# Kernel tuning notes

Measured on AMD Instinct MI355X. Metric: run time of the kernel, lower is better.

Reference implementation:

```python
import jax, jax.numpy as jnp
import numpy as np

Q, K, H, W, D, N, DFF = 48, 48, 24, 8, 512, 3, 2048
S = H * W  # 192
EPS = 1e-5
_BN_SCALE = np.float32(1.0 / np.sqrt(1.0 + EPS))  # eval-mode BN with rm=0, rv=1


def _bn(x, g, b):
    return x * (g * _BN_SCALE) + b


def _layer(tgt, mem, w1, b1, se, g1, bb1, w2, b2, g2, bb2, w3, b3, g3, bb3):
    # tgt: [q, S, D], mem: [k, S, D]
    query = tgt @ w1.T + b1
    key = mem @ w1.T + b1
    gate = jax.nn.sigmoid(se)  # [S, S]
    # large intermediate [q, k, s, t] -- the kernel-headroom hotspot
    score = jnp.einsum('qtd,ksd->qkst', query, key) * gate[None, None]
    qn, kn = tgt.shape[0], mem.shape[0]
    score = score.reshape(qn * kn, S, S)
    # dual max-pool, concatenated as [max_over_s, max_over_t] per pair
    x = jnp.stack([score.max(axis=1), score.max(axis=2)], axis=1).reshape(-1, S)  # [2qk, S]
    x = _bn(x, g1, bb1)
    x = _bn(x @ w2.T + b2, g2, bb2)
    x = jax.nn.relu(x)
    x = x @ w3.T + b3  # [2qk, 1]
    x = x.reshape(-1, 2).sum(axis=-1, keepdims=True)  # [qk, 1]
    x = _bn(x, g3, bb3)
    return x.reshape(qn, kn)


def setup_inputs() -> dict:
    key = jax.random.key(0)
    ks = jax.random.split(key, 16)
    se0 = jax.random.normal(ks[3], (N, S, S), jnp.float32)
    return {
        'memory': jax.random.normal(ks[0], (Q, H, W, D * N), jnp.float32),
        'features': jax.random.normal(ks[1], (K, H, W, D * N), jnp.float32),
        'fc1_w': jax.random.normal(ks[2], (N, D, D), jnp.float32) * np.float32(1.0 / np.sqrt(D)),
        'fc1_b': jnp.zeros((N, D), jnp.float32),
        'score_embed': se0 * np.float32(0.05),
        'bn1_g': 1.0 + 0.1 * jax.random.normal(ks[4], (N,), jnp.float32),
        'bn1_b': 0.1 * jax.random.normal(ks[5], (N,), jnp.float32),
        'fc2_w': jax.random.normal(ks[6], (N, DFF, S), jnp.float32) * np.float32(1.0 / np.sqrt(S)),
        'fc2_b': jnp.zeros((N, DFF), jnp.float32),
        'bn2_g': 1.0 + 0.1 * jax.random.normal(ks[7], (N, DFF), jnp.float32),
        'bn2_b': 0.1 * jax.random.normal(ks[8], (N, DFF), jnp.float32),
        'fc3_w': jax.random.normal(ks[9], (N, 1, DFF), jnp.float32) * np.float32(1.0 / np.sqrt(DFF)),
        'fc3_b': jnp.zeros((N, 1), jnp.float32),
        'bn3_g': 1.0 + 0.1 * jax.random.normal(ks[10], (N,), jnp.float32),
        'bn3_b': 0.1 * jax.random.normal(ks[11], (N,), jnp.float32),
        'norm_g': 1.0 + 0.1 * jax.random.normal(ks[12], (), jnp.float32),
        'norm_b': 0.1 * jax.random.normal(ks[13], (), jnp.float32),
    }


def reference(memory, features, fc1_w, fc1_b, score_embed, bn1_g, bn1_b,
              fc2_w, fc2_b, bn2_g, bn2_b, fc3_w, fc3_b, bn3_g, bn3_b,
              norm_g, norm_b):
    q, k = memory.shape[0], features.shape[0]
    # chunk(dim=-1) into N pieces of width D, then flatten h*w -> S
    tgt = memory.reshape(q, S, N, D)
    mem = features.reshape(k, S, N, D)
    score = jnp.zeros((q, k), jnp.float32)
    for i in range(N):
        score = score + _layer(tgt[:, :, i], mem[:, :, i],
                               fc1_w[i], fc1_b[i], score_embed[i],
                               bn1_g[i], bn1_b[i], fc2_w[i], fc2_b[i],
                               bn2_g[i], bn2_b[i], fc3_w[i], fc3_b[i],
                               bn3_g[i], bn3_b[i])
    # final decoder norm: BatchNorm1d(1) over flattened scores (eval mode)
    score = _bn(score, norm_g, norm_b)
    return score
```

## Files before the change

kernel.cpp:

```cpp
#include <hip/hip_runtime.h>
#include <math.h>

#define BN_SCALE 0.9999950000374997f

typedef unsigned short u16;
typedef short bfrag8 __attribute__((ext_vector_type(8)));
typedef float floatx4 __attribute__((ext_vector_type(4)));

struct ushort4_t { u16 x, y, z, w; };

__device__ __forceinline__ u16 f2bf(float f) {
  union { float f; unsigned u; } c; c.f = f;
  unsigned r = c.u + 0x7FFFu + ((c.u >> 16) & 1u);
  return (u16)(r >> 16);
}

__device__ __forceinline__ void gload_lds16(const u16* g, u16* l) {
  __builtin_amdgcn_global_load_lds(
      (const __attribute__((address_space(1))) void*)g,
      (__attribute__((address_space(3))) void*)l, 16, 0, 0);
}

__device__ __forceinline__ floatx4 mfma16(bfrag8 a, bfrag8 b, floatx4 c) {
  return __builtin_amdgcn_mfma_f32_16x16x32_bf16(a, b, c, 0, 0, 0);
}


__global__ void k_prep(const float* __restrict__ se, float* __restrict__ gateP,
                       const float* __restrict__ w2, const float* __restrict__ g2,
                       const float* __restrict__ b2, const float* __restrict__ bb2,
                       u16* __restrict__ w2B, float* __restrict__ beta2) {
  int idx = blockIdx.x * 256 + threadIdx.x;
  if (idx < 110592) {
    int e = idx & 3, lane = (idx >> 2) & 63;
    int rest = idx >> 8;
    int vq = rest % 36;
    int w = (rest / 36) & 3;
    int n = rest / 144;
    int i = vq / 6, j = vq - i * 6;
    int s = (w >> 1) * 96 + i * 16 + (lane >> 4) * 4 + e;
    int t = (w & 1) * 96 + j * 16 + (lane & 15);
    float x = se[n * 36864 + s * 192 + t];
    gateP[idx] = 1.0f / (1.0f + expf(-x));
    return;
  }
  idx -= 110592;
  if (idx < 1179648) {
    int nf = idx / 192;
    w2B[idx] = f2bf(w2[idx] * (g2[nf] * BN_SCALE));
    return;
  }
  idx -= 1179648;
  if (idx < 6144) beta2[idx] = b2[idx] * (g2[idx] * BN_SCALE) + bb2[idx];
}

__global__ __launch_bounds__(256, 2) void k_fc1(
    const float* __restrict__ memin, const float* __restrict__ featin,
    const float* __restrict__ w1, const float* __restrict__ b1,
    u16* __restrict__ qB, u16* __restrict__ kB) {
  __shared__ __align__(16) u16 At[128 * 64];
  __shared__ __align__(16) u16 Bt[128 * 64];
  const int tid = threadIdx.x, lane = tid & 63, wave = tid >> 6;
  const int bz = blockIdx.z, n = bz >> 1, side = bz & 1;
  const int m0 = blockIdx.y * 128, n0 = blockIdx.x * 128;
  const float* A = (side ? featin : memin) + n * 512;
  const float* B = w1 + (size_t)n * 262144;
  u16* Cn = (side ? kB : qB) + (size_t)n * 4718592;

  floatx4 acc[4][4];
  for (int i = 0; i < 4; i++)
    for (int j = 0; j < 4; j++) acc[i][j] = (floatx4){0.f, 0.f, 0.f, 0.f};
  const int wr = wave >> 1, wc = wave & 1;
  const int lr = lane & 15, lq = lane >> 4;
  const int sw = lr & 7;
  const int cc0 = (lq ^ sw) << 3, cc1 = ((lq + 4) ^ sw) << 3;

  for (int kk = 0; kk < 8; ++kk) {
    const int k0 = kk * 64;
    __syncthreads();
    for (int it = 0; it < 4; ++it) {
      int ch = it * 256 + tid;
      int row = ch >> 3, cc = ch & 7;
      int scc = cc ^ (row & 7);
      const float* srcA = &A[(size_t)(m0 + row) * 1536 + k0 + scc * 8];
      float4 a0 = *(const float4*)srcA;
      float4 a1 = *(const float4*)(srcA + 4);
      ushort4_t h0 = {f2bf(a0.x), f2bf(a0.y), f2bf(a0.z), f2bf(a0.w)};
      ushort4_t h1 = {f2bf(a1.x), f2bf(a1.y), f2bf(a1.z), f2bf(a1.w)};
      *(ushort4_t*)&At[ch * 8] = h0;
      *(ushort4_t*)&At[ch * 8 + 4] = h1;
      const float* srcB = &B[(size_t)(n0 + row) * 512 + k0 + scc * 8];
      float4 b0 = *(const float4*)srcB;
      float4 b1v = *(const float4*)(srcB + 4);
      ushort4_t g0 = {f2bf(b0.x), f2bf(b0.y), f2bf(b0.z), f2bf(b0.w)};
      ushort4_t g1 = {f2bf(b1v.x), f2bf(b1v.y), f2bf(b1v.z), f2bf(b1v.w)};
      *(ushort4_t*)&Bt[ch * 8] = g0;
      *(ushort4_t*)&Bt[ch * 8 + 4] = g1;
    }
    __syncthreads();
#pragma unroll
    for (int k2 = 0; k2 < 2; ++k2) {
      const int cco = k2 ? cc1 : cc0;
      bfrag8 a[4], b[4];
      for (int i = 0; i < 4; i++)
        a[i] = *(const bfrag8*)&At[(wr * 64 + i * 16 + lr) * 64 + cco];
      for (int j = 0; j < 4; j++)
        b[j] = *(const bfrag8*)&Bt[(wc * 64 + j * 16 + lr) * 64 + cco];
      for (int i = 0; i < 4; i++)
        for (int j = 0; j < 4; j++) acc[i][j] = mfma16(a[i], b[j], acc[i][j]);
    }
  }
  for (int j = 0; j < 4; j++) {
    int col = n0 + wc * 64 + j * 16 + lr;
    float bias = b1[n * 512 + col];
    int kkd = col >> 6, cw = col & 63;
    for (int i = 0; i < 4; i++) {
      int rbase = m0 + wr * 64 + i * 16 + lq * 4;
      for (int rg = 0; rg < 4; rg++) {
        int rr = rbase + rg;
        int tile = rr / 192, rw = rr - tile * 192;
        Cn[((size_t)tile * 8 + kkd) * 12288 + rw * 64 + cw] =
            f2bf(acc[i][j][rg] + bias);
      }
    }
  }
}

__global__ __launch_bounds__(256, 2) void k_score(
    const u16* __restrict__ qB, const u16* __restrict__ kB,
    const float* __restrict__ gateP,
    const float* __restrict__ bn1g, const float* __restrict__ bn1b,
    u16* __restrict__ pooled) {
  __shared__ __align__(16) u16 At[192 * 64];
  __shared__ __align__(16) u16 Bt[192 * 64];
  __shared__ float colL[8 * 192];
  __shared__ float rowL[2 * 192];
  const int tid = threadIdx.x, lane = tid & 63, wave = tid >> 6;
  const int lin = blockIdx.x, n = blockIdx.y;
  const int xcd = lin & 7, idx = lin >> 3;
  const int qIdx = idx / 6, kIdx = xcd * 6 + (idx - (idx / 6) * 6);
  const u16* A = kB + ((size_t)(n * 48 + kIdx) * 8) * 12288;
  const u16* Bp = qB + ((size_t)(n * 48 + qIdx) * 8) * 12288;
  const int ws = wave >> 1, wt = wave & 1;
  const int lr = lane & 15, lq = lane >> 4;
  const int sw = lr & 7;
  const int cc0 = (lq ^ sw) << 3;
  const int cc1 = ((lq + 4) ^ sw) << 3;

  floatx4 acc[6][6];
  for (int i = 0; i < 6; i++)
    for (int j = 0; j < 6; j++) acc[i][j] = (floatx4){0.f, 0.f, 0.f, 0.f};

  for (int kk = 0; kk < 8; ++kk) {
    const u16* Akk = A + kk * 12288;
    const u16* Bkk = Bp + kk * 12288;
    __syncthreads();
    for (int it = 0; it < 6; ++it) {
      int chb = it * 256 + wave * 64;
      int ch = chb + lane;
      int row = ch >> 3, cc = ch & 7;
      int src = (row << 3) + (cc ^ (row & 7));
      gload_lds16(Akk + src * 8, &At[chb * 8]);
      gload_lds16(Bkk + src * 8, &Bt[chb * 8]);
    }
    __syncthreads();
#pragma unroll
    for (int k2 = 0; k2 < 2; ++k2) {
      const int cco = k2 ? cc1 : cc0;
      bfrag8 a[6], b[6];
      for (int i = 0; i < 6; i++)
        a[i] = *(const bfrag8*)&At[(ws * 96 + i * 16 + lr) * 64 + cco];
      for (int j = 0; j < 6; j++)
        b[j] = *(const bfrag8*)&Bt[(wt * 96 + j * 16 + lr) * 64 + cco];
      for (int i = 0; i < 6; i++)
        for (int j = 0; j < 6; j++) acc[i][j] = mfma16(a[i], b[j], acc[i][j]);
    }
  }

  const float* gp = gateP + ((size_t)(n * 4 + wave) * 36) * 256 + lane * 4;
  float colp[6], rowp[6][4];
  for (int j = 0; j < 6; j++) colp[j] = -INFINITY;
  for (int i = 0; i < 6; i++)
    for (int rg = 0; rg < 4; rg++) rowp[i][rg] = -INFINITY;
  for (int i = 0; i < 6; i++) {
    for (int j = 0; j < 6; j++) {
      float4 g = *(const float4*)(gp + (i * 6 + j) * 256);
      const float* gv = (const float*)&g;
      for (int rg = 0; rg < 4; rg++) {
        float v = acc[i][j][rg] * gv[rg];
        colp[j] = fmaxf(colp[j], v);
        rowp[i][rg] = fmaxf(rowp[i][rg], v);
      }
    }
  }
  for (int j = 0; j < 6; j++)
    colL[(ws * 4 + lq) * 192 + wt * 96 + j * 16 + lr] = colp[j];
  for (int i = 0; i < 6; i++)
    for (int rg = 0; rg < 4; rg++) {
      float v = rowp[i][rg];
      v = fmaxf(v, __shfl_xor(v, 1));
      v = fmaxf(v, __shfl_xor(v, 2));
      v = fmaxf(v, __shfl_xor(v, 4));
      v = fmaxf(v, __shfl_xor(v, 8));
      if (lr == 0) rowL[wt * 192 + ws * 96 + i * 16 + lq * 4 + rg] = v;
    }
  __syncthreads();

  const float g1 = bn1g[n] * BN_SCALE;
  const float bb1 = bn1b[n];
  u16* outp = pooled + ((size_t)n * 2304 + (size_t)qIdx * 48 + kIdx) * 384;
  for (int id = tid; id < 384; id += 256) {
    if (id < 192) {
      float m = colL[id];
      for (int w = 1; w < 8; w++) m = fmaxf(m, colL[w * 192 + id]);
      outp[id] = f2bf(m * g1 + bb1);
    } else {
      int s = id - 192;
      float m = fmaxf(rowL[s], rowL[192 + s]);
      outp[id] = f2bf(m * g1 + bb1);
    }
  }
}

__global__ __launch_bounds__(256, 1) void k_mlp(
    const u16* __restrict__ pooled, const u16* __restrict__ w2B,
    const float* __restrict__ beta2, const float* __restrict__ w3,
    float* __restrict__ r) {
  __shared__ __align__(16) u16 Xt[128 * 64];
  __shared__ __align__(16) u16 Wt[128 * 64];
  const int tid = threadIdx.x, lane = tid & 63, wave = tid >> 6;
  const int n = blockIdx.z, row0 = blockIdx.y * 128, f0 = blockIdx.x * 512;
  const u16* X = pooled + ((size_t)n * 4608 + row0) * 192;
  const u16* W = w2B + (size_t)n * 2048 * 192;
  const int wr = wave >> 1, wc = wave & 1;
  const int lr = lane & 15, lq = lane >> 4;
  const int sw = lr & 7;
  const int cc0 = (lq ^ sw) << 3, cc1 = ((lq + 4) ^ sw) << 3;
  float rp[4][4];
  for (int i = 0; i < 4; i++)
    for (int rg = 0; rg < 4; rg++) rp[i][rg] = 0.f;

  for (int fs = 0; fs < 4; ++fs) {
    const int fb = f0 + fs * 128;
    floatx4 acc[4][4];
    for (int i = 0; i < 4; i++)
      for (int j = 0; j < 4; j++) acc[i][j] = (floatx4){0.f, 0.f, 0.f, 0.f};
    for (int kk = 0; kk < 3; ++kk) {
      const int k0 = kk * 64;
      __syncthreads();
      for (int it = 0; it < 4; ++it) {
        int chb = it * 256 + wave * 64;
        int ch = chb + lane;
        int row = ch >> 3, cc = ch & 7;
        int scc = (cc ^ (row & 7)) << 3;
        gload_lds16(X + (size_t)row * 192 + k0 + scc, &Xt[chb * 8]);
        gload_lds16(W + (size_t)(fb + row) * 192 + k0 + scc, &Wt[chb * 8]);
      }
      __syncthreads();
#pragma unroll
      for (int k2 = 0; k2 < 2; ++k2) {
        const int cco = k2 ? cc1 : cc0;
        bfrag8 a[4], b[4];
        for (int i = 0; i < 4; i++)
          a[i] = *(const bfrag8*)&Xt[(wr * 64 + i * 16 + lr) * 64 + cco];
        for (int j = 0; j < 4; j++)
          b[j] = *(const bfrag8*)&Wt[(wc * 64 + j * 16 + lr) * 64 + cco];
        for (int i = 0; i < 4; i++)
          for (int j = 0; j < 4; j++) acc[i][j] = mfma16(a[i], b[j], acc[i][j]);
      }
    }
    for (int j = 0; j < 4; j++) {
      int f = fb + wc * 64 + j * 16 + lr;
      float beta = beta2[n * 2048 + f];
      float w3f = w3[n * 2048 + f];
      for (int i = 0; i < 4; i++)
        for (int rg = 0; rg < 4; rg++) {
          float y = acc[i][j][rg] + beta;
          y = fmaxf(y, 0.f);
          rp[i][rg] += y * w3f;
        }
    }
  }
  for (int i = 0; i < 4; i++)
    for (int rg = 0; rg < 4; rg++) {
      float v = rp[i][rg];
      v += __shfl_xor(v, 1);
      v += __shfl_xor(v, 2);
      v += __shfl_xor(v, 4);
      v += __shfl_xor(v, 8);
      if (lr == 0) {
        int row = row0 + wr * 64 + i * 16 + lq * 4 + rg;
        atomicAdd(&r[n * 4608 + row], v);
      }
    }
}

__global__ void k_final(const float* __restrict__ r, const float* __restrict__ b3,
                        const float* __restrict__ g3, const float* __restrict__ bb3,
                        const float* __restrict__ ng, const float* __restrict__ nb,
                        float* __restrict__ out) {
  int p = blockIdx.x * 256 + threadIdx.x;
  if (p >= 2304) return;
  float acc = 0.f;
  for (int n = 0; n < 3; ++n) {
    float z = r[n * 4608 + 2 * p] + r[n * 4608 + 2 * p + 1] + 2.f * b3[n];
    acc += z * (g3[n] * BN_SCALE) + bb3[n];
  }
  out[p] = acc * (ng[0] * BN_SCALE) + nb[0];
}

extern "C" void kernel_launch(void* const* d_in, const int* in_sizes, int n_in,
                              void* d_out, int out_size, void* d_ws, size_t ws_size,
                              hipStream_t stream) {
  const float* memory = (const float*)d_in[0];
  const float* features = (const float*)d_in[1];
  const float* fc1_w = (const float*)d_in[2];
  const float* fc1_b = (const float*)d_in[3];
  const float* se = (const float*)d_in[4];
  const float* bn1_g = (const float*)d_in[5];
  const float* bn1_b = (const float*)d_in[6];
  const float* fc2_w = (const float*)d_in[7];
  const float* fc2_b = (const float*)d_in[8];
  const float* bn2_g = (const float*)d_in[9];
  const float* bn2_b = (const float*)d_in[10];
  const float* fc3_w = (const float*)d_in[11];
  const float* fc3_b = (const float*)d_in[12];
  const float* bn3_g = (const float*)d_in[13];
  const float* bn3_b = (const float*)d_in[14];
  const float* norm_g = (const float*)d_in[15];
  const float* norm_b = (const float*)d_in[16];

  char* ws = (char*)d_ws;
  float* gateP = (float*)ws;
  u16* w2B = (u16*)(ws + 442368);
  float* beta2 = (float*)(ws + 2801664);
  u16* qB = (u16*)(ws + 2826240);
  u16* kB = (u16*)(ws + 31137792);
  u16* pooled = (u16*)(ws + 59449344);
  float* r = (float*)(ws + 64757760);

  hipMemsetAsync(r, 0, 3 * 4608 * sizeof(float), stream);
  k_prep<<<dim3(5064), 256, 0, stream>>>(se, gateP, fc2_w, bn2_g, fc2_b, bn2_b,
                                         w2B, beta2);
  k_fc1<<<dim3(4, 72, 6), 256, 0, stream>>>(memory, features, fc1_w, fc1_b, qB, kB);
  k_score<<<dim3(2304, 3), 256, 0, stream>>>(qB, kB, gateP, bn1_g, bn1_b, pooled);
  k_mlp<<<dim3(4, 36, 3), 256, 0, stream>>>(pooled, w2B, beta2, fc3_w, r);
  k_final<<<dim3(9), 256, 0, stream>>>(r, fc3_b, bn3_g, bn3_b, norm_g, norm_b,
                                       (float*)d_out);
}
```

Measured before the change: 561.4 us.

## Pre-convert fc1 weights to bf16, stage fc1 output in LDS, split MLP grid

The fc1 weights are now converted to bf16 once in the prep kernel and loaded into LDS with direct global-to-LDS loads, so each fc1 block no longer reconverts them from fp32. The fc1 epilogue writes results into a swizzled LDS tile and then stores them with coalesced 16-byte writes instead of scattered 2-byte stores. The MLP kernel drops its inner loop over four feature slices, launching four times as many blocks with two blocks per CU allowed, which raises parallelism. The cost is an extra prep pass plus workspace for the weight copy, and more atomic adds into the result buffer.

```diff
diff --git a/kernel.cpp b/kernel.cpp
--- a/kernel.cpp
+++ b/kernel.cpp
@@ -27,6 +27,7 @@
 
 
 __global__ void k_prep(const float* __restrict__ se, float* __restrict__ gateP,
+                       const float* __restrict__ w1, u16* __restrict__ w1B,
                        const float* __restrict__ w2, const float* __restrict__ g2,
                        const float* __restrict__ b2, const float* __restrict__ bb2,
                        u16* __restrict__ w2B, float* __restrict__ beta2) {
@@ -45,6 +46,11 @@
     return;
   }
   idx -= 110592;
+  if (idx < 786432) {
+    w1B[idx] = f2bf(w1[idx]);
+    return;
+  }
+  idx -= 786432;
   if (idx < 1179648) {
     int nf = idx / 192;
     w2B[idx] = f2bf(w2[idx] * (g2[nf] * BN_SCALE));
@@ -56,15 +62,16 @@
 
 __global__ __launch_bounds__(256, 2) void k_fc1(
     const float* __restrict__ memin, const float* __restrict__ featin,
-    const float* __restrict__ w1, const float* __restrict__ b1,
+    const u16* __restrict__ w1B, const float* __restrict__ b1,
     u16* __restrict__ qB, u16* __restrict__ kB) {
-  __shared__ __align__(16) u16 At[128 * 64];
-  __shared__ __align__(16) u16 Bt[128 * 64];
+  __shared__ __align__(16) u16 T[128 * 128];
+  u16* At = T;
+  u16* Bt = T + 8192;
   const int tid = threadIdx.x, lane = tid & 63, wave = tid >> 6;
   const int bz = blockIdx.z, n = bz >> 1, side = bz & 1;
   const int m0 = blockIdx.y * 128, n0 = blockIdx.x * 128;
   const float* A = (side ? featin : memin) + n * 512;
-  const float* B = w1 + (size_t)n * 262144;
+  const u16* B = w1B + (size_t)n * 262144;
   u16* Cn = (side ? kB : qB) + (size_t)n * 4718592;
 
   floatx4 acc[4][4];
@@ -78,6 +85,13 @@
   for (int kk = 0; kk < 8; ++kk) {
     const int k0 = kk * 64;
     __syncthreads();
+    for (int it = 0; it < 4; ++it) {
+      int chb = it * 256 + wave * 64;
+      int ch = chb + lane;
+      int row = ch >> 3, cc = ch & 7;
+      int scc = cc ^ (row & 7);
+      gload_lds16(B + (size_t)(n0 + row) * 512 + k0 + scc * 8, &Bt[chb * 8]);
+    }
     for (int it = 0; it < 4; ++it) {
       int ch = it * 256 + tid;
       int row = ch >> 3, cc = ch & 7;
@@ -89,13 +103,6 @@
       ushort4_t h1 = {f2bf(a1.x), f2bf(a1.y), f2bf(a1.z), f2bf(a1.w)};
       *(ushort4_t*)&At[ch * 8] = h0;
       *(ushort4_t*)&At[ch * 8 + 4] = h1;
-      const float* srcB = &B[(size_t)(n0 + row) * 512 + k0 + scc * 8];
-      float4 b0 = *(const float4*)srcB;
-      float4 b1v = *(const float4*)(srcB + 4);
-      ushort4_t g0 = {f2bf(b0.x), f2bf(b0.y), f2bf(b0.z), f2bf(b0.w)};
-      ushort4_t g1 = {f2bf(b1v.x), f2bf(b1v.y), f2bf(b1v.z), f2bf(b1v.w)};
-      *(ushort4_t*)&Bt[ch * 8] = g0;
-      *(ushort4_t*)&Bt[ch * 8 + 4] = g1;
     }
     __syncthreads();
 #pragma unroll
@@ -110,19 +117,30 @@
         for (int j = 0; j < 4; j++) acc[i][j] = mfma16(a[i], b[j], acc[i][j]);
     }
   }
+
+  __syncthreads();
   for (int j = 0; j < 4; j++) {
-    int col = n0 + wc * 64 + j * 16 + lr;
-    float bias = b1[n * 512 + col];
-    int kkd = col >> 6, cw = col & 63;
+    int col = wc * 64 + j * 16 + lr;
+    float bias = b1[n * 512 + n0 + col];
+    int c = col >> 3, e = col & 7;
     for (int i = 0; i < 4; i++) {
-      int rbase = m0 + wr * 64 + i * 16 + lq * 4;
+      int rbase = wr * 64 + i * 16 + lq * 4;
       for (int rg = 0; rg < 4; rg++) {
-        int rr = rbase + rg;
-        int tile = rr / 192, rw = rr - tile * 192;
-        Cn[((size_t)tile * 8 + kkd) * 12288 + rw * 64 + cw] =
-            f2bf(acc[i][j][rg] + bias);
+        int row = rbase + rg;
+        T[row * 128 + (c ^ (row & 15)) * 8 + e] = f2bf(acc[i][j][rg] + bias);
       }
     }
+  }
+  __syncthreads();
+  for (int it = 0; it < 8; ++it) {
+    int ch = it * 256 + tid;
+    int row = ch >> 4, c = ch & 15;
+    int colg = n0 + c * 8;
+    int kkd = colg >> 6, cw = colg & 63;
+    int rr = m0 + row;
+    int tile = rr / 192, rw = rr - tile * 192;
+    *(uint4*)&Cn[((size_t)tile * 8 + kkd) * 12288 + rw * 64 + cw] =
+        *(const uint4*)&T[row * 128 + (c ^ (row & 15)) * 8];
   }
 }
 
@@ -222,64 +240,61 @@
   }
 }
 
-__global__ __launch_bounds__(256, 1) void k_mlp(
+__global__ __launch_bounds__(256, 2) void k_mlp(
     const u16* __restrict__ pooled, const u16* __restrict__ w2B,
     const float* __restrict__ beta2, const float* __restrict__ w3,
     float* __restrict__ r) {
   __shared__ __align__(16) u16 Xt[128 * 64];
   __shared__ __align__(16) u16 Wt[128 * 64];
   const int tid = threadIdx.x, lane = tid & 63, wave = tid >> 6;
-  const int n = blockIdx.z, row0 = blockIdx.y * 128, f0 = blockIdx.x * 512;
+  const int n = blockIdx.z, row0 = blockIdx.y * 128, fb = blockIdx.x * 128;
   const u16* X = pooled + ((size_t)n * 4608 + row0) * 192;
   const u16* W = w2B + (size_t)n * 2048 * 192;
   const int wr = wave >> 1, wc = wave & 1;
   const int lr = lane & 15, lq = lane >> 4;
   const int sw = lr & 7;
   const int cc0 = (lq ^ sw) << 3, cc1 = ((lq + 4) ^ sw) << 3;
+
+  floatx4 acc[4][4];
+  for (int i = 0; i < 4; i++)
+    for (int j = 0; j < 4; j++) acc[i][j] = (floatx4){0.f, 0.f, 0.f, 0.f};
+  for (int kk = 0; kk < 3; ++kk) {
+    const int k0 = kk * 64;
+    __syncthreads();
+    for (int it = 0; it < 4; ++it) {
+      int chb = it * 256 + wave * 64;
+      int ch = chb + lane;
+      int row = ch >> 3, cc = ch & 7;
+      int scc = (cc ^ (row & 7)) << 3;
+      gload_lds16(X + (size_t)row * 192 + k0 + scc, &Xt[chb * 8]);
+      gload_lds16(W + (size_t)(fb + row) * 192 + k0 + scc, &Wt[chb * 8]);
+    }
+    __syncthreads();
+#pragma unroll
+    for (int k2 = 0; k2 < 2; ++k2) {
+      const int cco = k2 ? cc1 : cc0;
+      bfrag8 a[4], b[4];
+      for (int i = 0; i < 4; i++)
+        a[i] = *(const bfrag8*)&Xt[(wr * 64 + i * 16 + lr) * 64 + cco];
+      for (int j = 0; j < 4; j++)
+        b[j] = *(const bfrag8*)&Wt[(wc * 64 + j * 16 + lr) * 64 + cco];
+      for (int i = 0; i < 4; i++)
+        for (int j = 0; j < 4; j++) acc[i][j] = mfma16(a[i], b[j], acc[i][j]);
+    }
+  }
   float rp[4][4];
   for (int i = 0; i < 4; i++)
     for (int rg = 0; rg < 4; rg++) rp[i][rg] = 0.f;
-
-  for (int fs = 0; fs < 4; ++fs) {
-    const int fb = f0 + fs * 128;
-    floatx4 acc[4][4];
+  for (int j = 0; j < 4; j++) {
+    int f = fb + wc * 64 + j * 16 + lr;
+    float beta = beta2[n * 2048 + f];
+    float w3f = w3[n * 2048 + f];
     for (int i = 0; i < 4; i++)
-      for (int j = 0; j < 4; j++) acc[i][j] = (floatx4){0.f, 0.f, 0.f, 0.f};
-    for (int kk = 0; kk < 3; ++kk) {
-      const int k0 = kk * 64;
-      __syncthreads();
-      for (int it = 0; it < 4; ++it) {
-        int chb = it * 256 + wave * 64;
-        int ch = chb + lane;
-        int row = ch >> 3, cc = ch & 7;
-        int scc = (cc ^ (row & 7)) << 3;
-        gload_lds16(X + (size_t)row * 192 + k0 + scc, &Xt[chb * 8]);
-        gload_lds16(W + (size_t)(fb + row) * 192 + k0 + scc, &Wt[chb * 8]);
+      for (int rg = 0; rg < 4; rg++) {
+        float y = acc[i][j][rg] + beta;
+        y = fmaxf(y, 0.f);
+        rp[i][rg] += y * w3f;
       }
-      __syncthreads();
-#pragma unroll
-      for (int k2 = 0; k2 < 2; ++k2) {
-        const int cco = k2 ? cc1 : cc0;
-        bfrag8 a[4], b[4];
-        for (int i = 0; i < 4; i++)
-          a[i] = *(const bfrag8*)&Xt[(wr * 64 + i * 16 + lr) * 64 + cco];
-        for (int j = 0; j < 4; j++)
-          b[j] = *(const bfrag8*)&Wt[(wc * 64 + j * 16 + lr) * 64 + cco];
-        for (int i = 0; i < 4; i++)
-          for (int j = 0; j < 4; j++) acc[i][j] = mfma16(a[i], b[j], acc[i][j]);
-      }
-    }
-    for (int j = 0; j < 4; j++) {
-      int f = fb + wc * 64 + j * 16 + lr;
-      float beta = beta2[n * 2048 + f];
-      float w3f = w3[n * 2048 + f];
-      for (int i = 0; i < 4; i++)
-        for (int rg = 0; rg < 4; rg++) {
-          float y = acc[i][j][rg] + beta;
-          y = fmaxf(y, 0.f);
-          rp[i][rg] += y * w3f;
-        }
-    }
   }
   for (int i = 0; i < 4; i++)
     for (int rg = 0; rg < 4; rg++) {
@@ -332,19 +347,20 @@
 
   char* ws = (char*)d_ws;
   float* gateP = (float*)ws;
-  u16* w2B = (u16*)(ws + 442368);
-  float* beta2 = (float*)(ws + 2801664);
-  u16* qB = (u16*)(ws + 2826240);
-  u16* kB = (u16*)(ws + 31137792);
-  u16* pooled = (u16*)(ws + 59449344);
-  float* r = (float*)(ws + 64757760);
+  u16* w1B = (u16*)(ws + 442368);
+  u16* w2B = (u16*)(ws + 2015232);
+  float* beta2 = (float*)(ws + 4374528);
+  u16* qB = (u16*)(ws + 4399104);
+  u16* kB = (u16*)(ws + 32710656);
+  u16* pooled = (u16*)(ws + 61022208);
+  float* r = (float*)(ws + 66330624);
 
   hipMemsetAsync(r, 0, 3 * 4608 * sizeof(float), stream);
-  k_prep<<<dim3(5064), 256, 0, stream>>>(se, gateP, fc2_w, bn2_g, fc2_b, bn2_b,
-                                         w2B, beta2);
-  k_fc1<<<dim3(4, 72, 6), 256, 0, stream>>>(memory, features, fc1_w, fc1_b, qB, kB);
+  k_prep<<<dim3(8136), 256, 0, stream>>>(se, gateP, fc1_w, w1B, fc2_w, bn2_g,
+                                         fc2_b, bn2_b, w2B, beta2);
+  k_fc1<<<dim3(4, 72, 6), 256, 0, stream>>>(memory, features, w1B, fc1_b, qB, kB);
   k_score<<<dim3(2304, 3), 256, 0, stream>>>(qB, kB, gateP, bn1_g, bn1_b, pooled);
-  k_mlp<<<dim3(4, 36, 3), 256, 0, stream>>>(pooled, w2B, beta2, fc3_w, r);
+  k_mlp<<<dim3(16, 36, 3), 256, 0, stream>>>(pooled, w2B, beta2, fc3_w, r);
   k_final<<<dim3(9), 256, 0, stream>>>(r, fc3_b, bn3_g, bn3_b, norm_g, norm_b,
                                        (float*)d_out);
 }
```

Result: faster. 499.8 us (-11.0%).
